# Optimization experiments

Measured on AMD Instinct MI355X. Metric: run time of the kernel, lower is better.

The kernel has to match this reference:

```python
import jax, jax.numpy as jnp
import numpy as np

B, N, CIN, K = 4, 4096, 64, 16
MLP = [64, 64, 128]
EPS = 1e-5


def setup_inputs() -> dict:
    key = jax.random.key(0)
    ks = jax.random.split(key, 8)
    inp = {
        "xyz": jax.random.normal(ks[0], (B, N, 3), dtype=jnp.float32),
        "points": jax.random.normal(ks[1], (B, N, CIN), dtype=jnp.float32),
    }
    last = 3 + CIN
    for i, oc in enumerate(MLP):
        inp[f"w{i}"] = jax.random.normal(ks[2 + i], (oc, last), dtype=jnp.float32) * 0.05
        inp[f"b{i}"] = jnp.zeros((oc,), dtype=jnp.float32)
        inp[f"g{i}"] = jnp.ones((oc,), dtype=jnp.float32)
        inp[f"be{i}"] = jnp.zeros((oc,), dtype=jnp.float32)
        inp[f"rm{i}"] = jnp.zeros((oc,), dtype=jnp.float32)
        inp[f"rv{i}"] = jnp.ones((oc,), dtype=jnp.float32)
        last = oc
    return inp


def reference(xyz, points, w0, b0, g0, be0, rm0, rv0,
              w1, b1, g1, be1, rm1, rv1,
              w2, b2, g2, be2, rm2, rv2):
    # knn via squared pairwise distance (same argsort order as cdist)
    sq = jnp.sum(xyz * xyz, axis=-1)  # (B,N)
    d2 = sq[:, :, None] + sq[:, None, :] - 2.0 * jnp.einsum('bnc,bmc->bnm', xyz, xyz)
    _, idx = jax.lax.top_k(-d2, K)  # (B,N,K), smallest-distance neighbors

    bidx = jnp.arange(xyz.shape[0])[:, None, None]  # (B,1,1)
    grouped_xyz = xyz[bidx, idx] - xyz[:, :, None, :]     # (B,N,K,3) relative coords
    grouped_pts = points[bidx, idx]                        # (B,N,K,CIN)
    h = jnp.concatenate([grouped_xyz, grouped_pts], axis=-1)  # (B,N,K,3+CIN)

    layers = [(w0, b0, g0, be0, rm0, rv0),
              (w1, b1, g1, be1, rm1, rv1),
              (w2, b2, g2, be2, rm2, rv2)]
    for (w, b, g, be, rm, rv) in layers:
        # 1x1 conv == per-point linear; BN in eval mode (running stats)
        h = jnp.einsum('bnkc,oc->bnko', h, w) + b
        h = (h - rm) * jax.lax.rsqrt(rv + EPS) * g + be
        h = jax.nn.relu(h)
    new_points = jnp.max(h, axis=2)  # max over K neighbors -> (B,N,C_out)
    return new_points
```

## Files before the change

### kernel.cpp

```cpp
#include <hip/hip_runtime.h>

#define NPT   4096
#define KNN_K 16
#define EPSV  1e-5f

#define W1T_OFF 4352
#define B1_OFF  8448
#define W2T_OFF 8512
#define B2_OFF  16704
#define IDX_OFF 16832
#define P_OFF   344512
#define Q_OFF   1393088

typedef unsigned long long ull;

__device__ __forceinline__ ull minu64(ull a, ull b) { return a < b ? a : b; }
__device__ __forceinline__ ull maxu64(ull a, ull b) { return a > b ? a : b; }

__device__ __forceinline__ ull bitonic_sort64(ull v, int lane) {
#pragma unroll
  for (int k = 2; k <= 64; k <<= 1) {
#pragma unroll
    for (int j = k >> 1; j > 0; j >>= 1) {
      ull o = __shfl_xor(v, j);
      bool lower = (lane & j) == 0;
      bool up = (lane & k) == 0;
      v = (lower == up) ? minu64(v, o) : maxu64(v, o);
    }
  }
  return v;
}

__device__ __forceinline__ ull bitonic_merge64(ull v, int lane) {
#pragma unroll
  for (int j = 32; j > 0; j >>= 1) {
    ull o = __shfl_xor(v, j);
    v = ((lane & j) == 0) ? minu64(v, o) : maxu64(v, o);
  }
  return v;
}

__device__ __forceinline__ void filter_step(float4 q, float4 c, unsigned idx32,
                                            unsigned& thresh_hi, int& cnt,
                                            ull& R, ull* buf, int lane) {
  float dot = __fadd_rn(__fadd_rn(__fmul_rn(q.x, c.x), __fmul_rn(q.y, c.y)),
                        __fmul_rn(q.z, c.z));
  float d2 = __fsub_rn(__fadd_rn(q.w, c.w), __fmul_rn(2.0f, dot));
  unsigned bits = __float_as_uint(d2);
  unsigned fk = bits ^ (0x80000000u | (unsigned)((int)bits >> 31));
  bool pred = fk <= thresh_hi;
  ull mask = __ballot(pred);
  if (mask) {
    int pos = cnt + (int)__builtin_amdgcn_mbcnt_hi(
                        (unsigned)(mask >> 32),
                        __builtin_amdgcn_mbcnt_lo((unsigned)mask, 0u));
    if (pred) buf[pos] = ((ull)fk << 32) | idx32;
    cnt += __popcll(mask);
    if (cnt >= 64) {
      ull v = buf[lane];
      v = bitonic_sort64(v, lane);
      ull vr = __shfl(v, 63 - lane);
      R = minu64(R, vr);
      R = bitonic_merge64(R, lane);
      thresh_hi = (unsigned)__shfl((int)(unsigned)(R >> 32), 15);
      cnt -= 64;
      if (lane < cnt) {
        ull tmp = buf[64 + lane];
        buf[lane] = tmp;
      }
    }
  }
}

__device__ __forceinline__ ull final_flush(ull R, int cnt, ull* buf, int lane) {
  ull v = (lane < cnt) ? buf[lane] : ~0ull;
  v = bitonic_sort64(v, lane);
  ull vr = __shfl(v, 63 - lane);
  R = minu64(R, vr);
  return bitonic_merge64(R, lane);
}

__global__ __launch_bounds__(256) void mega_kernel(
    const float* __restrict__ xyz, const float* __restrict__ points,
    const float* __restrict__ w0, const float* __restrict__ b0, const float* __restrict__ g0,
    const float* __restrict__ be0, const float* __restrict__ rm0, const float* __restrict__ rv0,
    const float* __restrict__ w1, const float* __restrict__ b1, const float* __restrict__ g1,
    const float* __restrict__ be1, const float* __restrict__ rm1, const float* __restrict__ rv1,
    const float* __restrict__ w2, const float* __restrict__ b2, const float* __restrict__ g2,
    const float* __restrict__ be2, const float* __restrict__ rm2, const float* __restrict__ rv2,
    float* __restrict__ ws, int* __restrict__ knnOut) {
  __shared__ __align__(16) unsigned char smem[20480];
  int blk = blockIdx.x;
  int tid = threadIdx.x;

  if (blk < 2048) {
    ull* bufb = (ull*)smem;
    int lane = tid & 63, w = tid >> 6;
    int b = blk >> 9;
    int n0 = ((blk & 511) << 3) + (w << 1);
    int n1 = n0 + 1;
    const float* xb = xyz + (size_t)b * NPT * 3;
    ull* buf0 = bufb + w * 256;
    ull* buf1 = buf0 + 128;

    float4 q0, q1;
    {
      const float* qp = xb + n0 * 3;
      float ax = qp[0], ay = qp[1], az = qp[2];
      float bx = qp[3], by = qp[4], bz = qp[5];
      q0 = make_float4(ax, ay, az,
          __fadd_rn(__fadd_rn(__fmul_rn(ax, ax), __fmul_rn(ay, ay)), __fmul_rn(az, az)));
      q1 = make_float4(bx, by, bz,
          __fadd_rn(__fadd_rn(__fmul_rn(bx, bx), __fmul_rn(by, by)), __fmul_rn(bz, bz)));
    }
    ull R0 = ~0ull, R1 = ~0ull;
    unsigned th0 = 0xFFFFFFFFu, th1 = 0xFFFFFFFFu;
    int cnt0 = 0, cnt1 = 0;

    float cx = xb[3 * lane], cy = xb[3 * lane + 1], cz = xb[3 * lane + 2];
#pragma unroll 1
    for (int g = 0; g < NPT; g += 64) {
      int ni = 3 * ((g + 64 + lane) & (NPT - 1));
      float nx = xb[ni], ny = xb[ni + 1], nz = xb[ni + 2];
      float csq = __fadd_rn(__fadd_rn(__fmul_rn(cx, cx), __fmul_rn(cy, cy)),
                            __fmul_rn(cz, cz));
      float4 c = make_float4(cx, cy, cz, csq);
      unsigned idx32 = (unsigned)(g + lane);
      filter_step(q0, c, idx32, th0, cnt0, R0, buf0, lane);
      filter_step(q1, c, idx32, th1, cnt1, R1, buf1, lane);
      cx = nx; cy = ny; cz = nz;
    }
    R0 = final_flush(R0, cnt0, buf0, lane);
    R1 = final_flush(R1, cnt1, buf1, lane);
    if (lane < KNN_K) {
      knnOut[(b * NPT + n0) * KNN_K + lane] = (int)(unsigned)(R0 & 0xFFFFFFFFull);
      knnOut[(b * NPT + n1) * KNN_K + lane] = (int)(unsigned)(R1 & 0xFFFFFFFFull);
    }
    return;
  }

  if (blk < 4096) {
    float* wlds = (float*)smem;
    for (int j = tid; j < 4288; j += 256) {
      int r = j / 67;
      float s = g0[r] * rsqrtf(rv0[r] + EPSV);
      wlds[j] = __fmul_rn(w0[j], s);
    }
    __syncthreads();
    int oc = tid & 63;
    int base = (blk - 2048) * 8 + (tid >> 6);
    float s = g0[oc] * rsqrtf(rv0[oc] + EPSV);
    float b0f = (b0[oc] - rm0[oc]) * s + be0[oc];
    const float* wrow = wlds + oc * 67;
#pragma unroll 1
    for (int pt = 0; pt < 2; ++pt) {
      int i = base + pt * 4;
      float x = xyz[i * 3], y = xyz[i * 3 + 1], z = xyz[i * 3 + 2];
      float qacc = wrow[0] * x;
      qacc = fmaf(wrow[1], y, qacc);
      qacc = fmaf(wrow[2], z, qacc);
      float acc = b0f + qacc;
      const float* prow = points + (size_t)i * 64;
#pragma unroll 4
      for (int c = 0; c < 64; ++c) acc = fmaf(wrow[3 + c], prow[c], acc);
      ws[P_OFF + (size_t)i * 64 + oc] = acc;
      ws[Q_OFF + (size_t)i * 64 + oc] = qacc;
    }
    return;
  }

  {
    int i = (blk - 4096) * 256 + tid + 4352;
    if (i < 8448) {
      int j = i - 4352; int oc = j & 63, ic = j >> 6;
      float s = g1[oc] * rsqrtf(rv1[oc] + EPSV);
      ws[i] = w1[oc * 64 + ic] * s;
    } else if (i < 8512) {
      int oc = i - 8448;
      float s = g1[oc] * rsqrtf(rv1[oc] + EPSV);
      ws[i] = (b1[oc] - rm1[oc]) * s + be1[oc];
    } else if (i < 16704) {
      int j = i - 8512; int ic = j >> 7, oc = j & 127;
      float s = g2[oc] * rsqrtf(rv2[oc] + EPSV);
      ws[i] = w2[oc * 64 + ic] * s;
    } else if (i < 16832) {
      int oc = i - 16704;
      float s = g2[oc] * rsqrtf(rv2[oc] + EPSV);
      ws[i] = (b2[oc] - rm2[oc]) * s + be2[oc];
    }
  }
}

__global__ __launch_bounds__(256, 4) void mlp_kernel(
    const float* __restrict__ wbuf, const int* __restrict__ knn,
    float* __restrict__ out) {
  __shared__ __align__(16) float Ash[64 * 128];
  __shared__ __align__(16) float Wsh[32 * 64];
  int tid = threadIdx.x;
  int qblk = blockIdx.x << 3;

  const float4* w1g = (const float4*)(wbuf + W1T_OFF);
  const float4* w2g = (const float4*)(wbuf + W2T_OFF);
  float4* wl = (float4*)Wsh;

#define W2IDX(e, p, h) ((((h) << 5) + ((e) >> 4)) * 32 + ((p) << 4) + ((e) & 15))

  float4 s0 = w1g[tid];
  float4 s1 = w1g[256 + tid];

  {
    int p = tid & 127, half = tid >> 7;
    int q = qblk + (p >> 4);
    int k = p & 15;
    int src = knn[q * KNN_K + k];
    int srow = (q & ~(NPT - 1)) + src;
    const float4* Pp = (const float4*)(wbuf + P_OFF + (size_t)srow * 64 + half * 32);
    const float4* Qp = (const float4*)(wbuf + Q_OFF + (size_t)q * 64 + half * 32);
#pragma unroll
    for (int j = 0; j < 8; ++j) {
      float4 pv = Pp[j];
      float4 qv = Qp[j];
      int ic = half * 32 + j * 4;
      Ash[(ic + 0) * 128 + p] = fmaxf(pv.x - qv.x, 0.0f);
      Ash[(ic + 1) * 128 + p] = fmaxf(pv.y - qv.y, 0.0f);
      Ash[(ic + 2) * 128 + p] = fmaxf(pv.z - qv.z, 0.0f);
      Ash[(ic + 3) * 128 + p] = fmaxf(pv.w - qv.w, 0.0f);
    }
  }
  wl[tid] = s0; wl[256 + tid] = s1;
  s0 = w1g[512 + tid]; s1 = w1g[768 + tid];
  __syncthreads();

  int og = tid & 7, pg = tid >> 3;
  const float* Arow = Ash + 4 * pg;
  const float* Wrow = Wsh + 8 * og;
  float acc[4][8];

#define GEMM32(R0)                                                        \
  _Pragma("unroll 8")                                                     \
  for (int ic = 0; ic < 32; ++ic) {                                       \
    float4 a0 = *(const float4*)(Arow + ((R0) + ic) * 128);               \
    float4 wv0 = *(const float4*)(Wrow + ic * 64);                        \
    float4 wv1 = *(const float4*)(Wrow + ic * 64 + 4);                    \
    float av[4] = {a0.x, a0.y, a0.z, a0.w};                               \
    float wv[8] = {wv0.x, wv0.y, wv0.z, wv0.w, wv1.x, wv1.y, wv1.z, wv1.w};\
    _Pragma("unroll")                                                     \
    for (int ii = 0; ii < 4; ++ii)                                        \
      _Pragma("unroll")                                                   \
      for (int jj = 0; jj < 8; ++jj) acc[ii][jj] = fmaf(av[ii], wv[jj], acc[ii][jj]); \
  }

  {
    float4 b0v = *(const float4*)(wbuf + B1_OFF + 8 * og);
    float4 b1v = *(const float4*)(wbuf + B1_OFF + 8 * og + 4);
    float bj[8] = {b0v.x, b0v.y, b0v.z, b0v.w, b1v.x, b1v.y, b1v.z, b1v.w};
#pragma unroll
    for (int i = 0; i < 4; ++i)
#pragma unroll
      for (int j = 0; j < 8; ++j) acc[i][j] = bj[j];
  }
  GEMM32(0)
  __syncthreads();
  wl[tid] = s0; wl[256 + tid] = s1;
  s0 = w2g[W2IDX(tid, 0, 0)]; s1 = w2g[W2IDX(tid + 256, 0, 0)];
  __syncthreads();
  GEMM32(32)
  __syncthreads();

#pragma unroll
  for (int j = 0; j < 8; ++j) {
    int oc = 8 * og + j;
    *(float4*)(Ash + oc * 128 + 4 * pg) =
        make_float4(fmaxf(acc[0][j], 0.0f), fmaxf(acc[1][j], 0.0f),
                    fmaxf(acc[2][j], 0.0f), fmaxf(acc[3][j], 0.0f));
  }
  wl[tid] = s0; wl[256 + tid] = s1;
  s0 = w2g[W2IDX(tid, 0, 1)]; s1 = w2g[W2IDX(tid + 256, 0, 1)];
  __syncthreads();

  int qout = qblk + (pg >> 2);
  float* obase = out + (size_t)qout * 128 + 8 * og;

  {
    float4 b0v = *(const float4*)(wbuf + B2_OFF + 8 * og);
    float4 b1v = *(const float4*)(wbuf + B2_OFF + 8 * og + 4);
    float bj[8] = {b0v.x, b0v.y, b0v.z, b0v.w, b1v.x, b1v.y, b1v.z, b1v.w};
#pragma unroll
    for (int i = 0; i < 4; ++i)
#pragma unroll
      for (int j = 0; j < 8; ++j) acc[i][j] = bj[j];
  }
  GEMM32(0)
  __syncthreads();
  wl[tid] = s0; wl[256 + tid] = s1;
  s0 = w2g[W2IDX(tid, 1, 0)]; s1 = w2g[W2IDX(tid + 256, 1, 0)];
  __syncthreads();
  GEMM32(32)
  {
    float m[8];
#pragma unroll
    for (int j = 0; j < 8; ++j) {
      float v = fmaxf(fmaxf(acc[0][j], acc[1][j]), fmaxf(acc[2][j], acc[3][j]));
      v = fmaxf(v, 0.0f);
      v = fmaxf(v, __shfl_xor(v, 8));
      m[j] = fmaxf(v, __shfl_xor(v, 16));
    }
    if ((pg & 3) == 0) {
      *(float4*)(obase)     = make_float4(m[0], m[1], m[2], m[3]);
      *(float4*)(obase + 4) = make_float4(m[4], m[5], m[6], m[7]);
    }
  }
  __syncthreads();
  wl[tid] = s0; wl[256 + tid] = s1;
  s0 = w2g[W2IDX(tid, 1, 1)]; s1 = w2g[W2IDX(tid + 256, 1, 1)];
  __syncthreads();

  {
    float4 b0v = *(const float4*)(wbuf + B2_OFF + 64 + 8 * og);
    float4 b1v = *(const float4*)(wbuf + B2_OFF + 64 + 8 * og + 4);
    float bj[8] = {b0v.x, b0v.y, b0v.z, b0v.w, b1v.x, b1v.y, b1v.z, b1v.w};
#pragma unroll
    for (int i = 0; i < 4; ++i)
#pragma unroll
      for (int j = 0; j < 8; ++j) acc[i][j] = bj[j];
  }
  GEMM32(0)
  __syncthreads();
  wl[tid] = s0; wl[256 + tid] = s1;
  __syncthreads();
  GEMM32(32)
  {
    float m[8];
#pragma unroll
    for (int j = 0; j < 8; ++j) {
      float v = fmaxf(fmaxf(acc[0][j], acc[1][j]), fmaxf(acc[2][j], acc[3][j]));
      v = fmaxf(v, 0.0f);
      v = fmaxf(v, __shfl_xor(v, 8));
      m[j] = fmaxf(v, __shfl_xor(v, 16));
    }
    if ((pg & 3) == 0) {
      *(float4*)(obase + 64)     = make_float4(m[0], m[1], m[2], m[3]);
      *(float4*)(obase + 64 + 4) = make_float4(m[4], m[5], m[6], m[7]);
    }
  }
#undef GEMM32
#undef W2IDX
}

extern "C" void kernel_launch(void* const* d_in, const int* in_sizes, int n_in,
                              void* d_out, int out_size, void* d_ws, size_t ws_size,
                              hipStream_t stream) {
  const float* xyz    = (const float*)d_in[0];
  const float* points = (const float*)d_in[1];
  float* wsF = (float*)d_ws;
  int* idxBuf = (int*)(wsF + IDX_OFF);

  mega_kernel<<<4145, 256, 0, stream>>>(
      xyz, points,
      (const float*)d_in[2],  (const float*)d_in[3],  (const float*)d_in[4],
      (const float*)d_in[5],  (const float*)d_in[6],  (const float*)d_in[7],
      (const float*)d_in[8],  (const float*)d_in[9],  (const float*)d_in[10],
      (const float*)d_in[11], (const float*)d_in[12], (const float*)d_in[13],
      (const float*)d_in[14], (const float*)d_in[15], (const float*)d_in[16],
      (const float*)d_in[17], (const float*)d_in[18], (const float*)d_in[19],
      wsF, idxBuf);
  mlp_kernel<<<2048, 256, 0, stream>>>(wsF, idxBuf, (float*)d_out);
}
```

Measured before the change: 238.9 us.

## Process four kNN queries per wavefront and software-pipeline the MLP GEMM loads

The kNN phase now has each wavefront handle four query points instead of two. Each candidate tile of xyz coordinates loaded from global memory is reused across more queries, which halves the kNN block count and shrinks the grid. Separately, the MLP GEMM inner loop is fully unrolled and double-buffers its LDS loads two iterations ahead, to hide LDS latency behind the FMAs. The cost is more register pressure, which could lower occupancy, and less parallelism in the kNN phase. The shared buffers now use the full 16 KB per block for kNN.

```diff
diff --git a/kernel.cpp b/kernel.cpp
--- a/kernel.cpp
+++ b/kernel.cpp
@@ -93,29 +93,36 @@
   int blk = blockIdx.x;
   int tid = threadIdx.x;
 
-  if (blk < 2048) {
+  if (blk < 1024) {
     ull* bufb = (ull*)smem;
     int lane = tid & 63, w = tid >> 6;
-    int b = blk >> 9;
-    int n0 = ((blk & 511) << 3) + (w << 1);
-    int n1 = n0 + 1;
+    int b = blk >> 8;
+    int n0 = ((blk & 255) << 4) + (w << 2);
     const float* xb = xyz + (size_t)b * NPT * 3;
-    ull* buf0 = bufb + w * 256;
+    ull* buf0 = bufb + w * 512;
     ull* buf1 = buf0 + 128;
-
-    float4 q0, q1;
+    ull* buf2 = buf0 + 256;
+    ull* buf3 = buf0 + 384;
+
+    float4 q0, q1, q2, q3;
     {
       const float* qp = xb + n0 * 3;
-      float ax = qp[0], ay = qp[1], az = qp[2];
-      float bx = qp[3], by = qp[4], bz = qp[5];
-      q0 = make_float4(ax, ay, az,
-          __fadd_rn(__fadd_rn(__fmul_rn(ax, ax), __fmul_rn(ay, ay)), __fmul_rn(az, az)));
-      q1 = make_float4(bx, by, bz,
-          __fadd_rn(__fadd_rn(__fmul_rn(bx, bx), __fmul_rn(by, by)), __fmul_rn(bz, bz)));
-    }
-    ull R0 = ~0ull, R1 = ~0ull;
-    unsigned th0 = 0xFFFFFFFFu, th1 = 0xFFFFFFFFu;
-    int cnt0 = 0, cnt1 = 0;
+      float x0 = qp[0], y0 = qp[1], z0 = qp[2];
+      float x1 = qp[3], y1 = qp[4], z1 = qp[5];
+      float x2 = qp[6], y2 = qp[7], z2 = qp[8];
+      float x3 = qp[9], y3 = qp[10], z3 = qp[11];
+      q0 = make_float4(x0, y0, z0,
+          __fadd_rn(__fadd_rn(__fmul_rn(x0, x0), __fmul_rn(y0, y0)), __fmul_rn(z0, z0)));
+      q1 = make_float4(x1, y1, z1,
+          __fadd_rn(__fadd_rn(__fmul_rn(x1, x1), __fmul_rn(y1, y1)), __fmul_rn(z1, z1)));
+      q2 = make_float4(x2, y2, z2,
+          __fadd_rn(__fadd_rn(__fmul_rn(x2, x2), __fmul_rn(y2, y2)), __fmul_rn(z2, z2)));
+      q3 = make_float4(x3, y3, z3,
+          __fadd_rn(__fadd_rn(__fmul_rn(x3, x3), __fmul_rn(y3, y3)), __fmul_rn(z3, z3)));
+    }
+    ull R0 = ~0ull, R1 = ~0ull, R2 = ~0ull, R3 = ~0ull;
+    unsigned th0 = 0xFFFFFFFFu, th1 = 0xFFFFFFFFu, th2 = 0xFFFFFFFFu, th3 = 0xFFFFFFFFu;
+    int cnt0 = 0, cnt1 = 0, cnt2 = 0, cnt3 = 0;
 
     float cx = xb[3 * lane], cy = xb[3 * lane + 1], cz = xb[3 * lane + 2];
 #pragma unroll 1
@@ -128,18 +135,24 @@
       unsigned idx32 = (unsigned)(g + lane);
       filter_step(q0, c, idx32, th0, cnt0, R0, buf0, lane);
       filter_step(q1, c, idx32, th1, cnt1, R1, buf1, lane);
+      filter_step(q2, c, idx32, th2, cnt2, R2, buf2, lane);
+      filter_step(q3, c, idx32, th3, cnt3, R3, buf3, lane);
       cx = nx; cy = ny; cz = nz;
     }
     R0 = final_flush(R0, cnt0, buf0, lane);
     R1 = final_flush(R1, cnt1, buf1, lane);
+    R2 = final_flush(R2, cnt2, buf2, lane);
+    R3 = final_flush(R3, cnt3, buf3, lane);
     if (lane < KNN_K) {
-      knnOut[(b * NPT + n0) * KNN_K + lane] = (int)(unsigned)(R0 & 0xFFFFFFFFull);
-      knnOut[(b * NPT + n1) * KNN_K + lane] = (int)(unsigned)(R1 & 0xFFFFFFFFull);
+      knnOut[(b * NPT + n0 + 0) * KNN_K + lane] = (int)(unsigned)(R0 & 0xFFFFFFFFull);
+      knnOut[(b * NPT + n0 + 1) * KNN_K + lane] = (int)(unsigned)(R1 & 0xFFFFFFFFull);
+      knnOut[(b * NPT + n0 + 2) * KNN_K + lane] = (int)(unsigned)(R2 & 0xFFFFFFFFull);
+      knnOut[(b * NPT + n0 + 3) * KNN_K + lane] = (int)(unsigned)(R3 & 0xFFFFFFFFull);
     }
     return;
   }
 
-  if (blk < 4096) {
+  if (blk < 3072) {
     float* wlds = (float*)smem;
     for (int j = tid; j < 4288; j += 256) {
       int r = j / 67;
@@ -148,7 +161,7 @@
     }
     __syncthreads();
     int oc = tid & 63;
-    int base = (blk - 2048) * 8 + (tid >> 6);
+    int base = (blk - 1024) * 8 + (tid >> 6);
     float s = g0[oc] * rsqrtf(rv0[oc] + EPSV);
     float b0f = (b0[oc] - rm0[oc]) * s + be0[oc];
     const float* wrow = wlds + oc * 67;
@@ -170,7 +183,7 @@
   }
 
   {
-    int i = (blk - 4096) * 256 + tid + 4352;
+    int i = (blk - 3072) * 256 + tid + 4352;
     if (i < 8448) {
       int j = i - 4352; int oc = j & 63, ic = j >> 6;
       float s = g1[oc] * rsqrtf(rv1[oc] + EPSV);
@@ -236,18 +249,28 @@
   const float* Wrow = Wsh + 8 * og;
   float acc[4][8];
 
+#define LD_A(R0, i)  (*(const float4*)(Arow + ((R0) + (i)) * 128))
+#define LD_W0(i)     (*(const float4*)(Wrow + (i) * 64))
+#define LD_W1(i)     (*(const float4*)(Wrow + (i) * 64 + 4))
 #define GEMM32(R0)                                                        \
-  _Pragma("unroll 8")                                                     \
-  for (int ic = 0; ic < 32; ++ic) {                                       \
-    float4 a0 = *(const float4*)(Arow + ((R0) + ic) * 128);               \
-    float4 wv0 = *(const float4*)(Wrow + ic * 64);                        \
-    float4 wv1 = *(const float4*)(Wrow + ic * 64 + 4);                    \
-    float av[4] = {a0.x, a0.y, a0.z, a0.w};                               \
-    float wv[8] = {wv0.x, wv0.y, wv0.z, wv0.w, wv1.x, wv1.y, wv1.z, wv1.w};\
+  {                                                                       \
+    float4 aA = LD_A(R0, 0), wA0 = LD_W0(0), wA1 = LD_W1(0);              \
+    float4 aB = LD_A(R0, 1), wB0 = LD_W0(1), wB1 = LD_W1(1);              \
     _Pragma("unroll")                                                     \
-    for (int ii = 0; ii < 4; ++ii)                                        \
+    for (int ic = 0; ic < 32; ++ic) {                                     \
+      int nx = (ic + 2 <= 31) ? ic + 2 : 31;                              \
+      float4 aN = LD_A(R0, nx);                                           \
+      float4 wN0 = LD_W0(nx);                                             \
+      float4 wN1 = LD_W1(nx);                                             \
+      float av[4] = {aA.x, aA.y, aA.z, aA.w};                             \
+      float wv[8] = {wA0.x, wA0.y, wA0.z, wA0.w, wA1.x, wA1.y, wA1.z, wA1.w};\
       _Pragma("unroll")                                                   \
-      for (int jj = 0; jj < 8; ++jj) acc[ii][jj] = fmaf(av[ii], wv[jj], acc[ii][jj]); \
+      for (int ii = 0; ii < 4; ++ii)                                      \
+        _Pragma("unroll")                                                 \
+        for (int jj = 0; jj < 8; ++jj) acc[ii][jj] = fmaf(av[ii], wv[jj], acc[ii][jj]); \
+      aA = aB; wA0 = wB0; wA1 = wB1;                                      \
+      aB = aN; wB0 = wN0; wB1 = wN1;                                      \
+    }                                                                     \
   }
 
   {
@@ -344,6 +367,9 @@
     }
   }
 #undef GEMM32
+#undef LD_A
+#undef LD_W0
+#undef LD_W1
 #undef W2IDX
 }
 
@@ -355,7 +381,7 @@
   float* wsF = (float*)d_ws;
   int* idxBuf = (int*)(wsF + IDX_OFF);
 
-  mega_kernel<<<4145, 256, 0, stream>>>(
+  mega_kernel<<<3121, 256, 0, stream>>>(
       xyz, points,
       (const float*)d_in[2],  (const float*)d_in[3],  (const float*)d_in[4],
       (const float*)d_in[5],  (const float*)d_in[6],  (const float*)d_in[7],
```

Result: no change. 243.2 us (+1.8%).
